# Optimization experiments

Hardware: AMD Instinct MI355X
Metric: run time of the kernel (lower is better)

Reference implementation:

```python
import jax, jax.numpy as jnp
import numpy as np

N, H, M, B = 512, 64, 1024, 256
ETA = 1.0
INIT_STD = 0.01

def setup_inputs() -> dict:
    key = jax.random.key(0)
    k1, k2, k3, k4 = jax.random.split(key, 4)
    # Binary +/-1 sequences and memory (as produced upstream in the repo)
    sequences = jnp.where(jax.random.uniform(k1, (B, N)) < 0.5, -1.0, 1.0).astype(jnp.float32)
    memory = jnp.where(jax.random.uniform(k2, (M, N)) < 0.5, -1.0, 1.0).astype(jnp.float32)
    A_logits = (INIT_STD * jax.random.normal(k3, (N, H, N))).astype(jnp.float32)
    B_logits = (INIT_STD * jax.random.normal(k4, (H, N))).astype(jnp.float32)
    return {"sequences": sequences, "memory": memory, "A_logits": A_logits, "B_logits": B_logits}

def reference(sequences, memory, A_logits, B_logits):
    # Vectorized version of DAM.train_batch's loss over positions n=1..N-1.
    n_dim = sequences.shape[1]
    # Causal mask: row for position n attends to indices i < n. Rows n=1..N-1.
    ns = jnp.arange(1, n_dim)[:, None, None]            # (N-1,1,1)
    idx = jnp.arange(n_dim)[None, None, :]              # (1,1,N)
    mask = idx < ns                                      # (N-1,1,N)
    neg_inf = jnp.asarray(-jnp.inf, A_logits.dtype)
    A = jax.nn.softmax(jnp.where(mask, A_logits[1:], neg_inf), axis=-1)  # (N-1,H,N), zeros outside mask
    Bn = jax.nn.softmax(B_logits, axis=-1)               # (H,N)
    phi_mu = jnp.einsum('hn,mn->mh', Bn, memory)         # (M,H) memory keys
    hat_phi = jnp.einsum('bi,nhi->bnh', sequences, A)    # (B,N-1,H) queries for every position at once
    score = ETA * jnp.einsum('bnh,mh->bnm', hat_phi, phi_mu)  # (B,N-1,M)
    pi = jax.nn.softmax(score, axis=-1)                  # retrieval distribution over memories
    plus = (memory[:, 1:] > 0).astype(pi.dtype)          # (M,N-1): memory bit at position n is +1
    prob = jnp.einsum('bnm,mn->bn', pi, plus)            # P(next bit = +1)
    prob = jnp.clip(prob, 1e-6, 1.0 - 1e-6)
    target = (sequences[:, 1:] > 0).astype(prob.dtype)
    bce = -(target * jnp.log(prob) + (1.0 - target) * jnp.log1p(-prob))
    # mean over batch per position, summed over positions, / (N-1) == global mean
    return jnp.mean(bce)
```

## Files before the change

### kernel.cpp

```cpp
#include <hip/hip_runtime.h>
#include <stdint.h>

#define NPOS 512
#define NH   64
#define NM   1024
#define NB   256
#define NM1  511

typedef __attribute__((ext_vector_type(8)))  short bf16x8;
typedef __attribute__((ext_vector_type(16))) float f32x16;
typedef __attribute__((ext_vector_type(4)))  float f32x4;
typedef __attribute__((ext_vector_type(4)))  int   i32x4;

#if __has_builtin(__builtin_amdgcn_exp2f)
#define EXP2F(x) __builtin_amdgcn_exp2f(x)
#else
#define EXP2F(x) __expf((x) * 0.69314718055994531f)
#endif

__device__ __forceinline__ unsigned short f2bf(float x) {
    unsigned u = __float_as_uint(x);
    u = (u + 0x7FFFu + ((u >> 16) & 1u)) >> 16;
    return (unsigned short)u;
}
__device__ __forceinline__ int pack2(unsigned short a, unsigned short b) {
    return (int)a | ((int)b << 16);
}
__device__ __forceinline__ int cvtpk(float lo, float hi) {
    int r;
    asm volatile("v_cvt_pk_bf16_f32 %0, %1, %2" : "=v"(r) : "v"(lo), "v"(hi));
    return r;
}

__global__ __launch_bounds__(256, 4)
void kA_prep(const float* __restrict__ seq, const float* __restrict__ Bl,
             const float* __restrict__ mem,
             unsigned short* __restrict__ seq_bf, float* __restrict__ BnT,
             float* __restrict__ plusT, float* __restrict__ out) {
    const int bid = blockIdx.x, t = threadIdx.x;
    if (bid < 128) {
        if (bid == 0 && t == 0) out[0] = 0.f;
        int idx = (bid * 256 + t) * 4;
        f32x4 v = *(const f32x4*)(seq + idx);
        int2 o;
        o.x = pack2(f2bf(v.x), f2bf(v.y));
        o.y = pack2(f2bf(v.z), f2bf(v.w));
        *(int2*)(seq_bf + idx) = o;
    } else if (bid < 144) {
        const int h = (bid - 128) * 4 + (t >> 6), l = t & 63;
        float v[8]; float mx = -1e30f;
#pragma unroll
        for (int j = 0; j < 8; j++) { v[j] = Bl[h * NPOS + l + 64 * j]; mx = fmaxf(mx, v[j]); }
#pragma unroll
        for (int o = 32; o; o >>= 1) mx = fmaxf(mx, __shfl_xor(mx, o));
        float s = 0.f;
#pragma unroll
        for (int j = 0; j < 8; j++) { v[j] = __expf(v[j] - mx); s += v[j]; }
#pragma unroll
        for (int o = 32; o; o >>= 1) s += __shfl_xor(s, o);
        float r = 1.0f / s;
#pragma unroll
        for (int j = 0; j < 8; j++) BnT[(l + 64 * j) * NH + h] = v[j] * r;
    } else {
        __shared__ float sT[64][65];
        const int bb = bid - 144;
        const int mt = bb >> 3, nt = bb & 7;
        const int rr = t >> 2, cc = t & 3;
        const float* src = mem + (size_t)(mt * 64 + rr) * NPOS + nt * 64 + cc * 16;
#pragma unroll
        for (int j = 0; j < 4; j++) {
            f32x4 v = *(const f32x4*)(src + j * 4);
            sT[rr][cc * 16 + j * 4 + 0] = (v.x > 0.f) ? 1.f : 0.f;
            sT[rr][cc * 16 + j * 4 + 1] = (v.y > 0.f) ? 1.f : 0.f;
            sT[rr][cc * 16 + j * 4 + 2] = (v.z > 0.f) ? 1.f : 0.f;
            sT[rr][cc * 16 + j * 4 + 3] = (v.w > 0.f) ? 1.f : 0.f;
        }
        __syncthreads();
        float* dst = plusT + (size_t)(nt * 64 + rr) * NM + mt * 64 + cc * 16;
#pragma unroll
        for (int j = 0; j < 4; j++) {
            f32x4 o;
            o.x = sT[cc * 16 + j * 4 + 0][rr];
            o.y = sT[cc * 16 + j * 4 + 1][rr];
            o.z = sT[cc * 16 + j * 4 + 2][rr];
            o.w = sT[cc * 16 + j * 4 + 3][rr];
            *(f32x4*)(dst + j * 4) = o;
        }
    }
}

__global__ __launch_bounds__(256, 4)
void k1b_phimu(const float* __restrict__ BnT, const float* __restrict__ mem,
               unsigned short* __restrict__ phimuF) {
    const int m0 = blockIdx.x * 8, t = threadIdx.x;
    __shared__ float mrow[8][NPOS];
    __shared__ float part[8][256];
#pragma unroll
    for (int ch = 0; ch < 4; ch++) {
        int idx = ch * 256 + t;
        int row = idx >> 7, col = (idx & 127) * 4;
        *(f32x4*)(&mrow[row][col]) = *(const f32x4*)(mem + (size_t)(m0 + row) * NPOS + col);
    }
    __syncthreads();
    const int h = t & 63, seg = t >> 6;
    float a[8], b2[8];
#pragma unroll
    for (int row = 0; row < 8; row++) { a[row] = 0.f; b2[row] = 0.f; }
    const float* bp = BnT + seg * 128 * NH + h;
#pragma unroll 4
    for (int nn = 0; nn < 128; nn += 2) {
        float x0 = bp[nn * NH], x1 = bp[(nn + 1) * NH];
#pragma unroll
        for (int row = 0; row < 8; row++) {
            a[row]  = fmaf(x0, mrow[row][seg * 128 + nn], a[row]);
            b2[row] = fmaf(x1, mrow[row][seg * 128 + nn + 1], b2[row]);
        }
    }
#pragma unroll
    for (int row = 0; row < 8; row++) part[row][t] = a[row] + b2[row];
    __syncthreads();
    if (t < 64) {
#pragma unroll
        for (int row = 0; row < 8; row++) {
            float s = (part[row][t] + part[row][t + 64]) + (part[row][t + 128] + part[row][t + 192]);
            unsigned short v = f2bf(s * 1.4426950408889634f);
            const int m = m0 + row;
            const int tile = m >> 5, rr = m & 31;
            const int kq = t >> 4, hi2 = (t >> 3) & 1, j = t & 7;
            phimuF[(size_t)((tile * 4 + kq) * 64 + rr + 32 * hi2) * 8 + j] = v;
        }
    }
}

__device__ __forceinline__ void p2_loadF(bf16x8 (&p)[4], const unsigned short* __restrict__ phimuF,
                                         int tile, int lane) {
#pragma unroll
    for (int kq = 0; kq < 4; kq++)
        p[kq] = *(const bf16x8*)(phimuF + (size_t)((tile * 4 + kq) * 64 + lane) * 8);
}

__global__ __launch_bounds__(256, 2)
void k23_fused(const float* __restrict__ Al, const unsigned short* __restrict__ seq_bf,
               const unsigned short* __restrict__ phimuF, const float* __restrict__ plusT,
               const float* __restrict__ seq, float* __restrict__ out) {
    __shared__ __align__(16) unsigned short e_lds[2][64 * 72];
    __shared__ __align__(16) unsigned short q_lds[256 * 72];
    __shared__ __align__(16) unsigned short plusbf[32 * 2 * 2 * 8];
    __shared__ float z_lds[64];
    __shared__ float w_lds[4];

    const int t = threadIdx.x;
    const int n = NM1 - (int)blockIdx.x;
    const int ksteps = (n + 63) >> 6;
    const int wv = t >> 6, lane = t & 63, half = lane >> 5, r = lane & 31;

    if (t < 64) z_lds[t] = 0.f;
    if (t < 128) {
        const int tile = t >> 2, mm = (t >> 1) & 1, hh = t & 1;
        const float* src = plusT + (size_t)n * NM + tile * 32 + mm * 16 + hh * 4;
        f32x4 v0 = *(const f32x4*)(src);
        f32x4 v1 = *(const f32x4*)(src + 8);
        unsigned short* dst = plusbf + (size_t)((tile * 2 + mm) * 2 + hh) * 8;
        dst[0] = f2bf(v0.x); dst[1] = f2bf(v0.y); dst[2] = f2bf(v0.z); dst[3] = f2bf(v0.w);
        dst[4] = f2bf(v1.x); dst[5] = f2bf(v1.y); dst[6] = f2bf(v1.z); dst[7] = f2bf(v1.w);
    }

    const int eh = t >> 2, ei = (t & 3) * 16;
    const float* arow = Al + ((size_t)n * NH + eh) * NPOS + ei;
    const unsigned short* s0 = seq_bf + (size_t)(wv * 64 + r) * NPOS;
    const unsigned short* s1 = seq_bf + (size_t)(wv * 64 + 32 + r) * NPOS;

    f32x16 acc00, acc01, acc10, acc11;
#pragma unroll
    for (int i = 0; i < 16; i++) { acc00[i] = 0.f; acc01[i] = 0.f; acc10[i] = 0.f; acc11[i] = 0.f; }

    f32x4 ea[4];
    bf16x8 sc0[4], sc1[4], sn0[4], sn1[4];
#pragma unroll
    for (int g = 0; g < 4; g++) ea[g] = *(const f32x4*)(arow + g * 4);
#pragma unroll
    for (int kq = 0; kq < 4; kq++) {
        sc0[kq] = *(const bf16x8*)(s0 + kq * 16 + half * 8);
        sc1[kq] = *(const bf16x8*)(s1 + kq * 16 + half * 8);
    }
    __syncthreads();

    for (int kk = 0; kk < ksteps; kk++) {
        const int k0 = kk * 64;
        unsigned short* ebuf = (unsigned short*)e_lds[kk & 1];
        {
            float zp = 0.f;
            unsigned short* ep = ebuf + eh * 72 + ei;
#pragma unroll
            for (int g = 0; g < 4; g++) {
                int i0 = k0 + ei + g * 4;
                float e0 = (i0 + 0 < n) ? __expf(ea[g].x) : 0.f;
                float e1 = (i0 + 1 < n) ? __expf(ea[g].y) : 0.f;
                float e2 = (i0 + 2 < n) ? __expf(ea[g].z) : 0.f;
                float e3 = (i0 + 3 < n) ? __expf(ea[g].w) : 0.f;
                zp += (e0 + e1) + (e2 + e3);
                int2 o; o.x = pack2(f2bf(e0), f2bf(e1)); o.y = pack2(f2bf(e2), f2bf(e3));
                *(int2*)(ep + g * 4) = o;
            }
            zp += __shfl_xor(zp, 1);
            zp += __shfl_xor(zp, 2);
            if ((t & 3) == 0) z_lds[eh] += zp;
        }
        if (kk + 1 < ksteps) {
#pragma unroll
            for (int g = 0; g < 4; g++) ea[g] = *(const f32x4*)(arow + k0 + 64 + g * 4);
#pragma unroll
            for (int kq = 0; kq < 4; kq++) {
                sn0[kq] = *(const bf16x8*)(s0 + k0 + 64 + kq * 16 + half * 8);
                sn1[kq] = *(const bf16x8*)(s1 + k0 + 64 + kq * 16 + half * 8);
            }
        }
        asm volatile("s_waitcnt lgkmcnt(0)" ::: "memory");
        __builtin_amdgcn_s_barrier();
        asm volatile("" ::: "memory");
        {
            const unsigned short* sB0 = ebuf + r * 72;
            const unsigned short* sB1 = sB0 + 32 * 72;
#pragma unroll
            for (int kq = 0; kq < 4; kq++) {
                const int ko = kq * 16 + half * 8;
                bf16x8 B0 = *(const bf16x8*)(sB0 + ko);
                bf16x8 B1 = *(const bf16x8*)(sB1 + ko);
                acc00 = __builtin_amdgcn_mfma_f32_32x32x16_bf16(sc0[kq], B0, acc00, 0, 0, 0);
                acc01 = __builtin_amdgcn_mfma_f32_32x32x16_bf16(sc0[kq], B1, acc01, 0, 0, 0);
                acc10 = __builtin_amdgcn_mfma_f32_32x32x16_bf16(sc1[kq], B0, acc10, 0, 0, 0);
                acc11 = __builtin_amdgcn_mfma_f32_32x32x16_bf16(sc1[kq], B1, acc11, 0, 0, 0);
            }
        }
        if (kk + 1 < ksteps) {
#pragma unroll
            for (int kq = 0; kq < 4; kq++) { sc0[kq] = sn0[kq]; sc1[kq] = sn1[kq]; }
        }
    }
    {
        float rz0 = 1.0f / z_lds[r];
        float rz1 = 1.0f / z_lds[32 + r];
#pragma unroll
        for (int reg = 0; reg < 16; reg++) {
            int row = (reg & 3) + 8 * (reg >> 2) + 4 * half;
            q_lds[(wv * 64 + row) * 72 + r]            = f2bf(acc00[reg] * rz0);
            q_lds[(wv * 64 + row) * 72 + 32 + r]       = f2bf(acc01[reg] * rz1);
            q_lds[(wv * 64 + 32 + row) * 72 + r]       = f2bf(acc10[reg] * rz0);
            q_lds[(wv * 64 + 32 + row) * 72 + 32 + r]  = f2bf(acc11[reg] * rz1);
        }
    }

    bf16x8 p[4], pn[4];
    p2_loadF(p, phimuF, 0, lane);
    bf16x8 q0[4], q1[4];
#pragma unroll
    for (int kq = 0; kq < 4; kq++) {
        q0[kq] = *(const bf16x8*)(q_lds + (wv * 64 + r) * 72 + kq * 16 + half * 8);
        q1[kq] = *(const bf16x8*)(q_lds + (wv * 64 + 32 + r) * 72 + kq * 16 + half * 8);
    }
    f32x16 zacc, accD0, accD1;
#pragma unroll
    for (int i = 0; i < 16; i++) { zacc[i] = 0.f; accD0[i] = 0.f; accD1[i] = 0.f; }

    const unsigned onespat = (r == 0) ? 0x3F803F80u : 0u;
    const unsigned pmask   = (r == 1) ? 0xFFFFFFFFu : 0u;

    for (int it = 0; it < 32; ++it) {
        if (it < 31) p2_loadF(pn, phimuF, it + 1, lane);
        f32x16 a0, a1;
        a0 = __builtin_amdgcn_mfma_f32_32x32x16_bf16(p[0], q0[0], zacc, 0, 0, 0);
        a1 = __builtin_amdgcn_mfma_f32_32x32x16_bf16(p[0], q1[0], zacc, 0, 0, 0);
#pragma unroll
        for (int kq = 1; kq < 4; kq++) {
            a0 = __builtin_amdgcn_mfma_f32_32x32x16_bf16(p[kq], q0[kq], a0, 0, 0, 0);
            a1 = __builtin_amdgcn_mfma_f32_32x32x16_bf16(p[kq], q1[kq], a1, 0, 0, 0);
        }
        i32x4 w1r = *(const i32x4*)(plusbf + (size_t)(4 * it + half) * 8);
        i32x4 w2r = *(const i32x4*)(plusbf + (size_t)(4 * it + 2 + half) * 8);
        i32x4 W1, W2;
        W1.x = onespat | (w1r.x & pmask); W1.y = onespat | (w1r.y & pmask);
        W1.z = onespat | (w1r.z & pmask); W1.w = onespat | (w1r.w & pmask);
        W2.x = onespat | (w2r.x & pmask); W2.y = onespat | (w2r.y & pmask);
        W2.z = onespat | (w2r.z & pmask); W2.w = onespat | (w2r.w & pmask);
        {
            float e00 = EXP2F(a0[0]),  e01 = EXP2F(a0[1]),  e02 = EXP2F(a0[2]),  e03 = EXP2F(a0[3]);
            float e04 = EXP2F(a0[4]),  e05 = EXP2F(a0[5]),  e06 = EXP2F(a0[6]),  e07 = EXP2F(a0[7]);
            float e08 = EXP2F(a0[8]),  e09 = EXP2F(a0[9]),  e10 = EXP2F(a0[10]), e11 = EXP2F(a0[11]);
            float e12 = EXP2F(a0[12]), e13 = EXP2F(a0[13]), e14 = EXP2F(a0[14]), e15 = EXP2F(a0[15]);
            i32x4 A1, A2;
            A1.x = cvtpk(e00, e01); A1.y = cvtpk(e02, e03); A1.z = cvtpk(e04, e05); A1.w = cvtpk(e06, e07);
            A2.x = cvtpk(e08, e09); A2.y = cvtpk(e10, e11); A2.z = cvtpk(e12, e13); A2.w = cvtpk(e14, e15);
            accD0 = __builtin_amdgcn_mfma_f32_32x32x16_bf16(*(bf16x8*)&A1, *(bf16x8*)&W1, accD0, 0, 0, 0);
            accD0 = __builtin_amdgcn_mfma_f32_32x32x16_bf16(*(bf16x8*)&A2, *(bf16x8*)&W2, accD0, 0, 0, 0);
        }
        {
            float e00 = EXP2F(a1[0]),  e01 = EXP2F(a1[1]),  e02 = EXP2F(a1[2]),  e03 = EXP2F(a1[3]);
            float e04 = EXP2F(a1[4]),  e05 = EXP2F(a1[5]),  e06 = EXP2F(a1[6]),  e07 = EXP2F(a1[7]);
            float e08 = EXP2F(a1[8]),  e09 = EXP2F(a1[9]),  e10 = EXP2F(a1[10]), e11 = EXP2F(a1[11]);
            float e12 = EXP2F(a1[12]), e13 = EXP2F(a1[13]), e14 = EXP2F(a1[14]), e15 = EXP2F(a1[15]);
            i32x4 A1, A2;
            A1.x = cvtpk(e00, e01); A1.y = cvtpk(e02, e03); A1.z = cvtpk(e04, e05); A1.w = cvtpk(e06, e07);
            A2.x = cvtpk(e08, e09); A2.y = cvtpk(e10, e11); A2.z = cvtpk(e12, e13); A2.w = cvtpk(e14, e15);
            accD1 = __builtin_amdgcn_mfma_f32_32x32x16_bf16(*(bf16x8*)&A1, *(bf16x8*)&W1, accD1, 0, 0, 0);
            accD1 = __builtin_amdgcn_mfma_f32_32x32x16_bf16(*(bf16x8*)&A2, *(bf16x8*)&W2, accD1, 0, 0, 0);
        }
        if (it < 31) {
#pragma unroll
            for (int kq = 0; kq < 4; kq++) p[kq] = pn[kq];
        }
    }

    __syncthreads();
    float* dsum = (float*)e_lds;
    float* nsum = dsum + 256;
    if (r < 2) {
        float* dst = (r == 0) ? dsum : nsum;
#pragma unroll
        for (int reg = 0; reg < 16; reg++) {
            int row = (reg & 3) + 8 * (reg >> 2) + 4 * half;
            dst[wv * 64 + row]      = accD0[reg];
            dst[wv * 64 + 32 + row] = accD1[reg];
        }
    }
    __syncthreads();
    {
        float dd = dsum[t], nn = nsum[t];
        float p2 = nn / dd;
        p2 = fminf(fmaxf(p2, 1e-6f), 1.0f - 1e-6f);
        float tg = seq[(size_t)t * NPOS + n];
        float bce = (tg > 0.f) ? -logf(p2) : -logf(1.0f - p2);
#pragma unroll
        for (int o = 32; o; o >>= 1) bce += __shfl_xor(bce, o);
        if (lane == 0) w_lds[wv] = bce;
    }
    __syncthreads();
    if (t == 0)
        atomicAdd(out, (w_lds[0] + w_lds[1] + w_lds[2] + w_lds[3]) * (1.0f / 130816.0f));
}

extern "C" void kernel_launch(void* const* d_in, const int* in_sizes, int n_in,
                              void* d_out, int out_size, void* d_ws, size_t ws_size,
                              hipStream_t stream) {
    const float* seq = (const float*)d_in[0];
    const float* mem = (const float*)d_in[1];
    const float* Al  = (const float*)d_in[2];
    const float* Bl  = (const float*)d_in[3];

    char* ws = (char*)d_ws;
    unsigned short* seq_bf = (unsigned short*)(ws + 0);
    float*          BnT    = (float*)(ws + 262144);
    unsigned short* phimuF = (unsigned short*)(ws + 393216);
    float*          plusT  = (float*)(ws + 524288);
    float*          outp   = (float*)d_out;

    kA_prep<<<272, 256, 0, stream>>>(seq, Bl, mem, seq_bf, BnT, plusT, outp);
    k1b_phimu<<<128, 256, 0, stream>>>(BnT, mem, phimuF);
    k23_fused<<<511, 256, 0, stream>>>(Al, seq_bf, phimuF, plusT, seq, outp);
}
```

Baseline: 142.1 us.

## Software-pipeline score MFMAs with exp conversion across memory tiles

Restructures the phase-2 loop into a two-stage ping-pong pipeline. While the exp2/bf16 conversion of one memory tile's scores runs on the VALU, the next tile's score MFMAs are issued, and the phi_mu loads are prefetched two tiles ahead. The aim is to overlap transcendental VALU work with matrix-core work, which the serial per-tile dependency chain prevented. It raises register pressure because two sets of score accumulators and operand buffers are live at once, under launch_bounds(256,2).

After: 143.6 us. Within noise of the previous version (+1.1%).

```diff
diff --git a/kernel.cpp b/kernel.cpp
--- a/kernel.cpp
+++ b/kernel.cpp
@@ -138,6 +138,51 @@
     for (int kq = 0; kq < 4; kq++)
         p[kq] = *(const bf16x8*)(phimuF + (size_t)((tile * 4 + kq) * 64 + lane) * 8);
 }
+__device__ __forceinline__ void p2_score(const bf16x8 (&p)[4], const bf16x8 (&q0)[4],
+                                         const bf16x8 (&q1)[4], const f32x16& zacc,
+                                         f32x16& a0, f32x16& a1) {
+    a0 = __builtin_amdgcn_mfma_f32_32x32x16_bf16(p[0], q0[0], zacc, 0, 0, 0);
+    a1 = __builtin_amdgcn_mfma_f32_32x32x16_bf16(p[0], q1[0], zacc, 0, 0, 0);
+#pragma unroll
+    for (int kq = 1; kq < 4; kq++) {
+        a0 = __builtin_amdgcn_mfma_f32_32x32x16_bf16(p[kq], q0[kq], a0, 0, 0, 0);
+        a1 = __builtin_amdgcn_mfma_f32_32x32x16_bf16(p[kq], q1[kq], a1, 0, 0, 0);
+    }
+}
+__device__ __forceinline__ void p2_expcvt(const f32x16& a0, const f32x16& a1,
+                                          i32x4& A1, i32x4& A2, i32x4& B1, i32x4& B2) {
+    {
+        float e00 = EXP2F(a0[0]),  e01 = EXP2F(a0[1]),  e02 = EXP2F(a0[2]),  e03 = EXP2F(a0[3]);
+        float e04 = EXP2F(a0[4]),  e05 = EXP2F(a0[5]),  e06 = EXP2F(a0[6]),  e07 = EXP2F(a0[7]);
+        float e08 = EXP2F(a0[8]),  e09 = EXP2F(a0[9]),  e10 = EXP2F(a0[10]), e11 = EXP2F(a0[11]);
+        float e12 = EXP2F(a0[12]), e13 = EXP2F(a0[13]), e14 = EXP2F(a0[14]), e15 = EXP2F(a0[15]);
+        A1.x = cvtpk(e00, e01); A1.y = cvtpk(e02, e03); A1.z = cvtpk(e04, e05); A1.w = cvtpk(e06, e07);
+        A2.x = cvtpk(e08, e09); A2.y = cvtpk(e10, e11); A2.z = cvtpk(e12, e13); A2.w = cvtpk(e14, e15);
+    }
+    {
+        float e00 = EXP2F(a1[0]),  e01 = EXP2F(a1[1]),  e02 = EXP2F(a1[2]),  e03 = EXP2F(a1[3]);
+        float e04 = EXP2F(a1[4]),  e05 = EXP2F(a1[5]),  e06 = EXP2F(a1[6]),  e07 = EXP2F(a1[7]);
+        float e08 = EXP2F(a1[8]),  e09 = EXP2F(a1[9]),  e10 = EXP2F(a1[10]), e11 = EXP2F(a1[11]);
+        float e12 = EXP2F(a1[12]), e13 = EXP2F(a1[13]), e14 = EXP2F(a1[14]), e15 = EXP2F(a1[15]);
+        B1.x = cvtpk(e00, e01); B1.y = cvtpk(e02, e03); B1.z = cvtpk(e04, e05); B1.w = cvtpk(e06, e07);
+        B2.x = cvtpk(e08, e09); B2.y = cvtpk(e10, e11); B2.z = cvtpk(e12, e13); B2.w = cvtpk(e14, e15);
+    }
+}
+__device__ __forceinline__ void p2_reduce(const i32x4& A1, const i32x4& A2,
+                                          const i32x4& B1, const i32x4& B2,
+                                          const i32x4& w1r, const i32x4& w2r,
+                                          unsigned onespat, unsigned pmask,
+                                          f32x16& accD0, f32x16& accD1) {
+    i32x4 W1, W2;
+    W1.x = onespat | (w1r.x & pmask); W1.y = onespat | (w1r.y & pmask);
+    W1.z = onespat | (w1r.z & pmask); W1.w = onespat | (w1r.w & pmask);
+    W2.x = onespat | (w2r.x & pmask); W2.y = onespat | (w2r.y & pmask);
+    W2.z = onespat | (w2r.z & pmask); W2.w = onespat | (w2r.w & pmask);
+    accD0 = __builtin_amdgcn_mfma_f32_32x32x16_bf16(*(const bf16x8*)&A1, *(const bf16x8*)&W1, accD0, 0, 0, 0);
+    accD0 = __builtin_amdgcn_mfma_f32_32x32x16_bf16(*(const bf16x8*)&A2, *(const bf16x8*)&W2, accD0, 0, 0, 0);
+    accD1 = __builtin_amdgcn_mfma_f32_32x32x16_bf16(*(const bf16x8*)&B1, *(const bf16x8*)&W1, accD1, 0, 0, 0);
+    accD1 = __builtin_amdgcn_mfma_f32_32x32x16_bf16(*(const bf16x8*)&B2, *(const bf16x8*)&W2, accD1, 0, 0, 0);
+}
 
 __global__ __launch_bounds__(256, 2)
 void k23_fused(const float* __restrict__ Al, const unsigned short* __restrict__ seq_bf,
@@ -250,8 +295,9 @@
         }
     }
 
-    bf16x8 p[4], pn[4];
-    p2_loadF(p, phimuF, 0, lane);
+    bf16x8 pA[4], pB[4];
+    p2_loadF(pA, phimuF, 0, lane);
+    p2_loadF(pB, phimuF, 1, lane);
     bf16x8 q0[4], q1[4];
 #pragma unroll
     for (int kq = 0; kq < 4; kq++) {
@@ -265,49 +311,24 @@
     const unsigned onespat = (r == 0) ? 0x3F803F80u : 0u;
     const unsigned pmask   = (r == 1) ? 0xFFFFFFFFu : 0u;
 
-    for (int it = 0; it < 32; ++it) {
-        if (it < 31) p2_loadF(pn, phimuF, it + 1, lane);
-        f32x16 a0, a1;
-        a0 = __builtin_amdgcn_mfma_f32_32x32x16_bf16(p[0], q0[0], zacc, 0, 0, 0);
-        a1 = __builtin_amdgcn_mfma_f32_32x32x16_bf16(p[0], q1[0], zacc, 0, 0, 0);
-#pragma unroll
-        for (int kq = 1; kq < 4; kq++) {
-            a0 = __builtin_amdgcn_mfma_f32_32x32x16_bf16(p[kq], q0[kq], a0, 0, 0, 0);
-            a1 = __builtin_amdgcn_mfma_f32_32x32x16_bf16(p[kq], q1[kq], a1, 0, 0, 0);
-        }
-        i32x4 w1r = *(const i32x4*)(plusbf + (size_t)(4 * it + half) * 8);
-        i32x4 w2r = *(const i32x4*)(plusbf + (size_t)(4 * it + 2 + half) * 8);
-        i32x4 W1, W2;
-        W1.x = onespat | (w1r.x & pmask); W1.y = onespat | (w1r.y & pmask);
-        W1.z = onespat | (w1r.z & pmask); W1.w = onespat | (w1r.w & pmask);
-        W2.x = onespat | (w2r.x & pmask); W2.y = onespat | (w2r.y & pmask);
-        W2.z = onespat | (w2r.z & pmask); W2.w = onespat | (w2r.w & pmask);
-        {
-            float e00 = EXP2F(a0[0]),  e01 = EXP2F(a0[1]),  e02 = EXP2F(a0[2]),  e03 = EXP2F(a0[3]);
-            float e04 = EXP2F(a0[4]),  e05 = EXP2F(a0[5]),  e06 = EXP2F(a0[6]),  e07 = EXP2F(a0[7]);
-            float e08 = EXP2F(a0[8]),  e09 = EXP2F(a0[9]),  e10 = EXP2F(a0[10]), e11 = EXP2F(a0[11]);
-            float e12 = EXP2F(a0[12]), e13 = EXP2F(a0[13]), e14 = EXP2F(a0[14]), e15 = EXP2F(a0[15]);
-            i32x4 A1, A2;
-            A1.x = cvtpk(e00, e01); A1.y = cvtpk(e02, e03); A1.z = cvtpk(e04, e05); A1.w = cvtpk(e06, e07);
-            A2.x = cvtpk(e08, e09); A2.y = cvtpk(e10, e11); A2.z = cvtpk(e12, e13); A2.w = cvtpk(e14, e15);
-            accD0 = __builtin_amdgcn_mfma_f32_32x32x16_bf16(*(bf16x8*)&A1, *(bf16x8*)&W1, accD0, 0, 0, 0);
-            accD0 = __builtin_amdgcn_mfma_f32_32x32x16_bf16(*(bf16x8*)&A2, *(bf16x8*)&W2, accD0, 0, 0, 0);
-        }
-        {
-            float e00 = EXP2F(a1[0]),  e01 = EXP2F(a1[1]),  e02 = EXP2F(a1[2]),  e03 = EXP2F(a1[3]);
-            float e04 = EXP2F(a1[4]),  e05 = EXP2F(a1[5]),  e06 = EXP2F(a1[6]),  e07 = EXP2F(a1[7]);
-            float e08 = EXP2F(a1[8]),  e09 = EXP2F(a1[9]),  e10 = EXP2F(a1[10]), e11 = EXP2F(a1[11]);
-            float e12 = EXP2F(a1[12]), e13 = EXP2F(a1[13]), e14 = EXP2F(a1[14]), e15 = EXP2F(a1[15]);
-            i32x4 A1, A2;
-            A1.x = cvtpk(e00, e01); A1.y = cvtpk(e02, e03); A1.z = cvtpk(e04, e05); A1.w = cvtpk(e06, e07);
-            A2.x = cvtpk(e08, e09); A2.y = cvtpk(e10, e11); A2.z = cvtpk(e12, e13); A2.w = cvtpk(e14, e15);
-            accD1 = __builtin_amdgcn_mfma_f32_32x32x16_bf16(*(bf16x8*)&A1, *(bf16x8*)&W1, accD1, 0, 0, 0);
-            accD1 = __builtin_amdgcn_mfma_f32_32x32x16_bf16(*(bf16x8*)&A2, *(bf16x8*)&W2, accD1, 0, 0, 0);
-        }
-        if (it < 31) {
-#pragma unroll
-            for (int kq = 0; kq < 4; kq++) p[kq] = pn[kq];
-        }
+    f32x16 aA0, aA1, aB0, aB1;
+    p2_score(pA, q0, q1, zacc, aA0, aA1);
+
+    for (int it = 0; it < 32; it += 2) {
+        i32x4 wA1 = *(const i32x4*)(plusbf + (size_t)(4 * it + half) * 8);
+        i32x4 wA2 = *(const i32x4*)(plusbf + (size_t)(4 * it + 2 + half) * 8);
+        if (it + 2 < 32) p2_loadF(pA, phimuF, it + 2, lane);
+        i32x4 EA1, EA2, EB1, EB2;
+        p2_expcvt(aA0, aA1, EA1, EA2, EB1, EB2);
+        p2_score(pB, q0, q1, zacc, aB0, aB1);
+        p2_reduce(EA1, EA2, EB1, EB2, wA1, wA2, onespat, pmask, accD0, accD1);
+        i32x4 wB1 = *(const i32x4*)(plusbf + (size_t)(4 * (it + 1) + half) * 8);
+        i32x4 wB2 = *(const i32x4*)(plusbf + (size_t)(4 * (it + 1) + 2 + half) * 8);
+        if (it + 3 < 32) p2_loadF(pB, phimuF, it + 3, lane);
+        i32x4 FA1, FA2, FB1, FB2;
+        p2_expcvt(aB0, aB1, FA1, FA2, FB1, FB2);
+        if (it + 2 < 32) p2_score(pA, q0, q1, zacc, aA0, aA1);
+        p2_reduce(FA1, FA2, FB1, FB2, wB1, wB2, onespat, pmask, accD0, accD1);
     }
 
     __syncthreads();
```

## Pair long and short positions per block order, pad LDS rows, precompute weight operands

Applied to the files above, without the earlier changes.

Block indices are remapped so consecutive blocks alternate between the longest and shortest causal positions, which should even out per-CU work as blocks are scheduled. LDS row stride drops from 72 to 66 halfwords to change the bank mapping for the e/q tiles. The per-iteration mask/OR construction of the plus-weight MFMA operand is replaced by reading precomputed ones/zeros/plus rows through per-lane pointers. The odd stride of 66 halfwords misaligns the 16-byte bf16x8 LDS loads, which could split accesses or break alignment assumptions.

After: 150.1 us. +5.6%, slower.

```diff
diff --git a/kernel.cpp b/kernel.cpp
--- a/kernel.cpp
+++ b/kernel.cpp
@@ -6,6 +6,7 @@
 #define NM   1024
 #define NB   256
 #define NM1  511
+#define LDW  66
 
 typedef __attribute__((ext_vector_type(8)))  short bf16x8;
 typedef __attribute__((ext_vector_type(16))) float f32x16;
@@ -143,14 +144,15 @@
 void k23_fused(const float* __restrict__ Al, const unsigned short* __restrict__ seq_bf,
                const unsigned short* __restrict__ phimuF, const float* __restrict__ plusT,
                const float* __restrict__ seq, float* __restrict__ out) {
-    __shared__ __align__(16) unsigned short e_lds[2][64 * 72];
-    __shared__ __align__(16) unsigned short q_lds[256 * 72];
-    __shared__ __align__(16) unsigned short plusbf[32 * 2 * 2 * 8];
+    __shared__ __align__(16) unsigned short e_lds[2][64 * LDW];
+    __shared__ __align__(16) unsigned short q_lds[256 * LDW];
+    __shared__ __align__(16) unsigned short plusbf[1040];
     __shared__ float z_lds[64];
     __shared__ float w_lds[4];
 
     const int t = threadIdx.x;
-    const int n = NM1 - (int)blockIdx.x;
+    const int c0 = blockIdx.x >> 1;
+    const int n = (blockIdx.x & 1) ? (1 + c0) : (NM1 - c0);
     const int ksteps = (n + 63) >> 6;
     const int wv = t >> 6, lane = t & 63, half = lane >> 5, r = lane & 31;
 
@@ -163,6 +165,9 @@
         unsigned short* dst = plusbf + (size_t)((tile * 2 + mm) * 2 + hh) * 8;
         dst[0] = f2bf(v0.x); dst[1] = f2bf(v0.y); dst[2] = f2bf(v0.z); dst[3] = f2bf(v0.w);
         dst[4] = f2bf(v1.x); dst[5] = f2bf(v1.y); dst[6] = f2bf(v1.z); dst[7] = f2bf(v1.w);
+    } else if (t == 128) {
+#pragma unroll
+        for (int j = 0; j < 8; j++) { plusbf[1024 + j] = 0x3F80; plusbf[1032 + j] = 0; }
     }
 
     const int eh = t >> 2, ei = (t & 3) * 16;
@@ -190,7 +195,7 @@
         unsigned short* ebuf = (unsigned short*)e_lds[kk & 1];
         {
             float zp = 0.f;
-            unsigned short* ep = ebuf + eh * 72 + ei;
+            unsigned short* ep = ebuf + eh * LDW + ei;
 #pragma unroll
             for (int g = 0; g < 4; g++) {
                 int i0 = k0 + ei + g * 4;
@@ -219,8 +224,8 @@
         __builtin_amdgcn_s_barrier();
         asm volatile("" ::: "memory");
         {
-            const unsigned short* sB0 = ebuf + r * 72;
-            const unsigned short* sB1 = sB0 + 32 * 72;
+            const unsigned short* sB0 = ebuf + r * LDW;
+            const unsigned short* sB1 = sB0 + 32 * LDW;
 #pragma unroll
             for (int kq = 0; kq < 4; kq++) {
                 const int ko = kq * 16 + half * 8;
@@ -243,10 +248,10 @@
 #pragma unroll
         for (int reg = 0; reg < 16; reg++) {
             int row = (reg & 3) + 8 * (reg >> 2) + 4 * half;
-            q_lds[(wv * 64 + row) * 72 + r]            = f2bf(acc00[reg] * rz0);
-            q_lds[(wv * 64 + row) * 72 + 32 + r]       = f2bf(acc01[reg] * rz1);
-            q_lds[(wv * 64 + 32 + row) * 72 + r]       = f2bf(acc10[reg] * rz0);
-            q_lds[(wv * 64 + 32 + row) * 72 + 32 + r]  = f2bf(acc11[reg] * rz1);
+            q_lds[(wv * 64 + row) * LDW + r]            = f2bf(acc00[reg] * rz0);
+            q_lds[(wv * 64 + row) * LDW + 32 + r]       = f2bf(acc01[reg] * rz1);
+            q_lds[(wv * 64 + 32 + row) * LDW + r]       = f2bf(acc10[reg] * rz0);
+            q_lds[(wv * 64 + 32 + row) * LDW + 32 + r]  = f2bf(acc11[reg] * rz1);
         }
     }
 
@@ -255,15 +260,18 @@
     bf16x8 q0[4], q1[4];
 #pragma unroll
     for (int kq = 0; kq < 4; kq++) {
-        q0[kq] = *(const bf16x8*)(q_lds + (wv * 64 + r) * 72 + kq * 16 + half * 8);
-        q1[kq] = *(const bf16x8*)(q_lds + (wv * 64 + 32 + r) * 72 + kq * 16 + half * 8);
+        q0[kq] = *(const bf16x8*)(q_lds + (wv * 64 + r) * LDW + kq * 16 + half * 8);
+        q1[kq] = *(const bf16x8*)(q_lds + (wv * 64 + 32 + r) * LDW + kq * 16 + half * 8);
     }
     f32x16 zacc, accD0, accD1;
 #pragma unroll
     for (int i = 0; i < 16; i++) { zacc[i] = 0.f; accD0[i] = 0.f; accD1[i] = 0.f; }
 
-    const unsigned onespat = (r == 0) ? 0x3F803F80u : 0u;
-    const unsigned pmask   = (r == 1) ? 0xFFFFFFFFu : 0u;
+    const unsigned short* wb1 = (r == 1) ? (plusbf + half * 8)
+                              : (r == 0) ? (plusbf + 1024) : (plusbf + 1032);
+    const unsigned short* wb2 = (r == 1) ? (plusbf + (2 + half) * 8)
+                              : (r == 0) ? (plusbf + 1024) : (plusbf + 1032);
+    const int wstep = (r == 1) ? 32 : 0;
 
     for (int it = 0; it < 32; ++it) {
         if (it < 31) p2_loadF(pn, phimuF, it + 1, lane);
@@ -275,13 +283,9 @@
             a0 = __builtin_amdgcn_mfma_f32_32x32x16_bf16(p[kq], q0[kq], a0, 0, 0, 0);
             a1 = __builtin_amdgcn_mfma_f32_32x32x16_bf16(p[kq], q1[kq], a1, 0, 0, 0);
         }
-        i32x4 w1r = *(const i32x4*)(plusbf + (size_t)(4 * it + half) * 8);
-        i32x4 w2r = *(const i32x4*)(plusbf + (size_t)(4 * it + 2 + half) * 8);
-        i32x4 W1, W2;
-        W1.x = onespat | (w1r.x & pmask); W1.y = onespat | (w1r.y & pmask);
-        W1.z = onespat | (w1r.z & pmask); W1.w = onespat | (w1r.w & pmask);
-        W2.x = onespat | (w2r.x & pmask); W2.y = onespat | (w2r.y & pmask);
-        W2.z = onespat | (w2r.z & pmask); W2.w = onespat | (w2r.w & pmask);
+        i32x4 W1 = *(const i32x4*)wb1;
+        i32x4 W2 = *(const i32x4*)wb2;
+        wb1 += wstep; wb2 += wstep;
         {
             float e00 = EXP2F(a0[0]),  e01 = EXP2F(a0[1]),  e02 = EXP2F(a0[2]),  e03 = EXP2F(a0[3]);
             float e04 = EXP2F(a0[4]),  e05 = EXP2F(a0[5]),  e06 = EXP2F(a0[6]),  e07 = EXP2F(a0[7]);
```
